# Kernel tuning notes

Hardware: AMD Instinct MI355X
Metric: run time of the kernel (lower is better)

Reference implementation:

```python
import jax, jax.numpy as jnp
import numpy as np

N_NODES = 100000
NODES_PER_GRAPH = 200
N_GRAPHS = N_NODES // NODES_PER_GRAPH  # 500
N_EDGES = 3200000
NUM_FEATURES = 128
HIDDEN = 32
K_POOL = 50
NUM_CLASSES = 10
NUM_ITERATIONS = 3


def setup_inputs() -> dict:
    key = jax.random.key(0)
    ks = jax.random.split(key, 12)
    x = jax.random.normal(ks[0], (N_NODES, NUM_FEATURES), dtype=jnp.float32)
    edge_index = jax.random.randint(ks[1], (2, N_EDGES), 0, N_NODES, dtype=jnp.int64)
    batch = (jnp.arange(N_NODES, dtype=jnp.int64) // NODES_PER_GRAPH)
    # GCN weights (glorot-ish scale) + biases
    W1 = jax.random.normal(ks[2], (NUM_FEATURES, HIDDEN), dtype=jnp.float32) * (1.0 / np.sqrt(NUM_FEATURES))
    b1 = jnp.zeros((HIDDEN,), dtype=jnp.float32)
    W2 = jax.random.normal(ks[3], (HIDDEN, HIDDEN), dtype=jnp.float32) * (1.0 / np.sqrt(HIDDEN))
    b2 = jnp.zeros((HIDDEN,), dtype=jnp.float32)
    W3 = jax.random.normal(ks[4], (HIDDEN, HIDDEN), dtype=jnp.float32) * (1.0 / np.sqrt(HIDDEN))
    b3 = jnp.zeros((HIDDEN,), dtype=jnp.float32)
    # Capsule weights: [out_capsules, in_capsules, out_length, in_length]
    Wc1 = jax.random.normal(ks[5], (16, K_POOL, 32, 3 * HIDDEN), dtype=jnp.float32) * 0.05
    Wc2 = jax.random.normal(ks[6], (NUM_CLASSES, 16, 16, 32), dtype=jnp.float32) * 0.05
    return {"x": x, "edge_index": edge_index, "batch": batch,
            "W1": W1, "b1": b1, "W2": W2, "b2": b2, "W3": W3, "b3": b3,
            "Wc1": Wc1, "Wc2": Wc2}


def _gcn_conv(x, W, b, src, dst, mask):
    # PyG GCNConv: remove self-loops already done (mask), add self-loops, sym-normalize.
    h = x @ W  # [N, H]
    deg = jnp.zeros((x.shape[0],), dtype=h.dtype).at[dst].add(mask) + 1.0  # self-loop adds 1
    dinv = jax.lax.rsqrt(deg)
    norm = dinv[src] * dinv[dst] * mask  # [E]
    agg = jnp.zeros_like(h).at[dst].add(norm[:, None] * h[src])
    agg = agg + h * (dinv * dinv)[:, None]  # self-loop contribution h_i / deg_i
    return agg + b


def _squash(s, axis=-1):
    sq = jnp.sum(s * s, axis=axis, keepdims=True)
    return (sq / (1.0 + sq)) * s * jax.lax.rsqrt(sq + 1e-12)


def _capsule_linear(u, W, num_iterations):
    # u: [B, I, in_len]; W: [O, I, out_len, in_len]
    priors = jnp.einsum('oiLl,bil->boiL', W, u)  # [B, O, I, out_len]
    logits = jnp.zeros(priors.shape[:3] + (1,), dtype=priors.dtype)
    for it in range(num_iterations):
        c = jax.nn.softmax(logits, axis=1)             # over out capsules
        s = jnp.sum(c * priors, axis=2)                # [B, O, out_len]
        v = _squash(s)
        if it < num_iterations - 1:
            logits = logits + jnp.sum(priors * v[:, :, None, :], axis=-1, keepdims=True)
    return v


def _global_sort_pool(x, k):
    # x: [N, C], equal-size graphs -> [B, nper, C]; sort desc by last channel, take top-k
    xg = x.reshape(N_GRAPHS, NODES_PER_GRAPH, x.shape[-1])
    order = jnp.argsort(-xg[:, :, -1], axis=1)[:, :k]  # [B, k]
    return jnp.take_along_axis(xg, order[:, :, None], axis=1)  # [B, k, C]


def reference(x, edge_index, batch, W1, b1, W2, b2, W3, b3, Wc1, Wc2):
    src, dst = edge_index[0], edge_index[1]
    mask = (src != dst).astype(x.dtype)  # remove_self_loops
    x1 = jnp.tanh(_gcn_conv(x, W1, b1, src, dst, mask))
    x2 = jnp.tanh(_gcn_conv(x1, W2, b2, src, dst, mask))
    x3 = jnp.tanh(_gcn_conv(x2, W3, b3, src, dst, mask))
    xc = jnp.concatenate([x1, x2, x3], axis=-1)        # [N, 96]
    pooled = _global_sort_pool(xc, K_POOL)             # [B, 50, 96]
    out = _capsule_linear(pooled, Wc1, NUM_ITERATIONS)  # [B, 16, 32]
    out = _capsule_linear(out, Wc2, NUM_ITERATIONS)     # [B, 10, 16]
    return jnp.linalg.norm(out, axis=-1)                # [B, 10]
```

## Files before the change

kernel.cpp:

```cpp
#include <hip/hip_runtime.h>

#define NNODES 100000
#define NEDGES 3200000
#define NPG 200
#define NGRAPH 500
#define FIN 128
#define HID 32
#define KP 50
#define NCLS 10

#define NB1 196
#define BSH 9
#define CHUNK 8192
#define NBLK1 391
#define CAP 17408

__global__ __launch_bounds__(512) void k_place1(const int* __restrict__ src,
                                                const int* __restrict__ dst,
                                                int* __restrict__ cursor,
                                                unsigned* __restrict__ csorted) {
    __shared__ int hist[NB1];
    __shared__ int lstart[NB1];
    __shared__ int base[NB1];
    __shared__ int cnt2[NB1];
    __shared__ int sarr[256];
    __shared__ unsigned buf[CHUNK];
    __shared__ int dbuf[CHUNK];
    int t = threadIdx.x;
    for (int i = t; i < NB1; i += 512) { hist[i] = 0; cnt2[i] = 0; }
    __syncthreads();
    int eb = blockIdx.x * CHUNK;
    for (int i = 0; i < CHUNK / 512; ++i) {
        int e = eb + t + i * 512;
        if (e < NEDGES) {
            int s = src[e], d = dst[e];
            if (s != d) atomicAdd(&hist[d >> BSH], 1);
        }
    }
    __syncthreads();
    if (t < 256) sarr[t] = (t < NB1) ? hist[t] : 0;
    __syncthreads();
    for (int ofs = 1; ofs < 256; ofs <<= 1) {
        int add = (t < 256 && t >= ofs) ? sarr[t - ofs] : 0;
        __syncthreads();
        if (t < 256) sarr[t] += add;
        __syncthreads();
    }
    if (t < NB1) {
        lstart[t] = (t == 0) ? 0 : sarr[t - 1];
        base[t] = hist[t] ? (t * CAP + atomicAdd(&cursor[t], hist[t])) : 0;
    }
    __syncthreads();
    for (int i = 0; i < CHUNK / 512; ++i) {
        int e = eb + t + i * 512;
        if (e < NEDGES) {
            int s = src[e], d = dst[e];
            if (s != d) {
                int bk = d >> BSH;
                int pos = atomicAdd(&cnt2[bk], 1);
                int slot = lstart[bk] + pos;
                buf[slot] = ((unsigned)s << BSH) | (unsigned)(d & 511);
                dbuf[slot] = base[bk] + pos;
            }
        }
    }
    __syncthreads();
    int nval = sarr[NB1 - 1];
    for (int j = t; j < nval; j += 512) csorted[dbuf[j]] = buf[j];
}

__global__ __launch_bounds__(512) void k_fill2(const int* __restrict__ cursor,
                                               const unsigned* __restrict__ csorted,
                                               int* __restrict__ csrc,
                                               int2* __restrict__ begend,
                                               float* __restrict__ dinv) {
    __shared__ int cnt[512];
    __shared__ int loffs[512];
    __shared__ int cnt2[512];
    __shared__ int sarr[512];
    int b = blockIdx.x, t = threadIdx.x;
    cnt[t] = 0; cnt2[t] = 0;
    __syncthreads();
    int base = b * CAP;
    int m = cursor[b];
    for (int j = t; j < m; j += 512) atomicAdd(&cnt[csorted[base + j] & 511], 1);
    __syncthreads();
    sarr[t] = cnt[t];
    __syncthreads();
    for (int ofs = 1; ofs < 512; ofs <<= 1) {
        int add = (t >= ofs) ? sarr[t - ofs] : 0;
        __syncthreads();
        sarr[t] += add;
        __syncthreads();
    }
    loffs[t] = sarr[t] - cnt[t];
    __syncthreads();
    int n = b * 512 + t;
    if (n < NNODES) {
        int beg = base + loffs[t];
        begend[n] = make_int2(beg, beg + cnt[t]);
        dinv[n] = rsqrtf((float)cnt[t] + 1.0f);
    }
    for (int j = t; j < m; j += 512) {
        unsigned p = csorted[base + j];
        int d = p & 511;
        int pos = atomicAdd(&cnt2[d], 1);
        csrc[base + loffs[d] + pos] = (int)(p >> BSH);
    }
}

__global__ __launch_bounds__(256) void k_matmul(const float* __restrict__ X, int ldx, int K,
                                                const float* __restrict__ W,
                                                const float* __restrict__ dinv,
                                                float* __restrict__ h) {
    __shared__ float Wl[FIN * HID];
    __shared__ float Xl[64 * FIN];
    int t = threadIdx.x;
    for (int idx = t; idx < K * HID; idx += 256) Wl[idx] = W[idx];
    int n0 = blockIdx.x * 64;
    int ng = 64 * K / 4;
    for (int idx = t; idx < ng; idx += 256) {
        int r = (idx * 4) / K, c = (idx * 4) % K;
        float4 v = make_float4(0.f, 0.f, 0.f, 0.f);
        if (n0 + r < NNODES)
            v = *reinterpret_cast<const float4*>(X + (size_t)(n0 + r) * ldx + c);
        *reinterpret_cast<float4*>(&Xl[r * K + c]) = v;
    }
    __syncthreads();
    int j = t & 31, g = t >> 5;
    const float* xr = &Xl[(g * 8) * K];
    float a0 = 0, a1 = 0, a2 = 0, a3 = 0, a4 = 0, a5 = 0, a6 = 0, a7 = 0;
    for (int k = 0; k < K; ++k) {
        float w = Wl[k * HID + j];
        a0 += w * xr[0 * K + k];
        a1 += w * xr[1 * K + k];
        a2 += w * xr[2 * K + k];
        a3 += w * xr[3 * K + k];
        a4 += w * xr[4 * K + k];
        a5 += w * xr[5 * K + k];
        a6 += w * xr[6 * K + k];
        a7 += w * xr[7 * K + k];
    }
    int r0 = n0 + g * 8;
    float av[8] = {a0, a1, a2, a3, a4, a5, a6, a7};
    for (int q = 0; q < 8; ++q)
        if (r0 + q < NNODES) h[(size_t)(r0 + q) * HID + j] = av[q] * dinv[r0 + q];
}

__global__ __launch_bounds__(256) void k_gather(const int2* __restrict__ begend,
                                                const int* __restrict__ csrc,
                                                const float* __restrict__ dinv,
                                                const float* __restrict__ hw,
                                                const float* __restrict__ bias,
                                                float* __restrict__ xc, int coloff) {
    int t = threadIdx.x;
    int wv = t >> 6;
    int lane = t & 63;
    int nh = lane >> 5;
    int sub = lane & 31;
    int g = sub >> 3;
    int q = sub & 7;
    int n = blockIdx.x * 8 + wv * 2 + nh;
    int2 be = begend[n];
    int beg = be.x, end = be.y, last = end - 1;
    float4 acc = make_float4(0.f, 0.f, 0.f, 0.f);
    for (int e0 = beg + g; e0 < end; e0 += 32) {
#pragma unroll
        for (int j = 0; j < 8; ++j) {
            int e = e0 + 4 * j;
            float mk = (e <= last) ? 1.f : 0.f;
            int s = csrc[min(e, last)];
            float4 hv = *reinterpret_cast<const float4*>(hw + (size_t)s * HID + q * 4);
            acc.x += mk * hv.x; acc.y += mk * hv.y; acc.z += mk * hv.z; acc.w += mk * hv.w;
        }
    }
    for (int m = 8; m <= 16; m <<= 1) {
        acc.x += __shfl_xor(acc.x, m, 64);
        acc.y += __shfl_xor(acc.y, m, 64);
        acc.z += __shfl_xor(acc.z, m, 64);
        acc.w += __shfl_xor(acc.w, m, 64);
    }
    if (g == 0) {
        float di = dinv[n];
        float4 hv = *reinterpret_cast<const float4*>(hw + (size_t)n * HID + q * 4);
        float4 bv = *reinterpret_cast<const float4*>(bias + q * 4);
        float4 v;
        v.x = tanhf(di * (acc.x + hv.x) + bv.x);
        v.y = tanhf(di * (acc.y + hv.y) + bv.y);
        v.z = tanhf(di * (acc.z + hv.z) + bv.z);
        v.w = tanhf(di * (acc.w + hv.w) + bv.w);
        *reinterpret_cast<float4*>(xc + (size_t)n * 96 + coloff + q * 4) = v;
    }
}

__global__ __launch_bounds__(256) void k_sortpool(const float* __restrict__ xc,
                                                  float* __restrict__ pooled) {
    int g = blockIdx.x;
    __shared__ float vals[NPG];
    __shared__ int sel[KP];
    int t = threadIdx.x;
    if (t < NPG) vals[t] = xc[((size_t)g * NPG + t) * 96 + 95];
    __syncthreads();
    if (t < NPG) {
        float v = vals[t];
        int r = 0;
        for (int k = 0; k < NPG; ++k) {
            float vk = vals[k];
            r += (vk > v) || (vk == v && k < t);
        }
        if (r < KP) sel[r] = t;
    }
    __syncthreads();
    for (int idx = t; idx < KP * 24; idx += 256) {
        int r = idx / 24, c4 = (idx % 24) * 4;
        *reinterpret_cast<float4*>(pooled + (size_t)g * KP * 96 + r * 96 + c4) =
            *reinterpret_cast<const float4*>(xc + ((size_t)g * NPG + sel[r]) * 96 + c4);
    }
}

__global__ __launch_bounds__(256) void k_priors1(const float* __restrict__ pooled,
                                                 const float* __restrict__ Wc1,
                                                 float* __restrict__ priors) {
    int bid = blockIdx.x;
    int ct = bid & 3;
    int bt = (bid >> 2) & 3;
    int i = bid >> 4;
    __shared__ float As[48 * 128];
    __shared__ float Bs[48 * 128];
    int t = threadIdx.x;
    int tx = t & 15, ty = t >> 4;
    float4 accL[8], accH[8];
#pragma unroll
    for (int r = 0; r < 8; ++r) {
        accL[r] = make_float4(0.f, 0.f, 0.f, 0.f);
        accH[r] = make_float4(0.f, 0.f, 0.f, 0.f);
    }

    for (int kh = 0; kh < 2; ++kh) {
        int kbase = kh * 48;
        __syncthreads();
        for (int idx = t; idx < 128 * 12; idx += 256) {
            int r = idx / 12, c4 = (idx % 12) * 4;
            int b = bt * 128 + r;
            float4 v = make_float4(0.f, 0.f, 0.f, 0.f);
            if (b < NGRAPH)
                v = *reinterpret_cast<const float4*>(pooled + ((size_t)b * KP + i) * 96 + kbase + c4);
            float vv[4] = {v.x, v.y, v.z, v.w};
#pragma unroll
            for (int j = 0; j < 4; ++j) {
                int k = c4 + j;
                int gp = (r >> 2) ^ ((k >> 2) & 31);
                As[k * 128 + gp * 4 + (r & 3)] = vv[j];
            }
        }
        for (int idx = t; idx < 128 * 12; idx += 256) {
            int c = idx / 12, c4 = (idx % 12) * 4;
            int col = ct * 128 + c;
            const float* wr = Wc1 + (((size_t)(col >> 5) * KP + i) * 32 + (col & 31)) * 96;
            float4 v = *reinterpret_cast<const float4*>(wr + kbase + c4);
            float vv[4] = {v.x, v.y, v.z, v.w};
#pragma unroll
            for (int j = 0; j < 4; ++j) {
                int k = c4 + j;
                int gp = (c >> 2) ^ ((k >> 2) & 31);
                Bs[k * 128 + gp * 4 + (c & 3)] = vv[j];
            }
        }
        __syncthreads();
        for (int k = 0; k < 48; ++k) {
            int key = (k >> 2) & 31;
            float4 a0 = *reinterpret_cast<const float4*>(&As[k * 128 + 4 * ((2 * ty) ^ key)]);
            float4 a1 = *reinterpret_cast<const float4*>(&As[k * 128 + 4 * ((2 * ty + 1) ^ key)]);
            float4 b0 = *reinterpret_cast<const float4*>(&Bs[k * 128 + 4 * ((2 * tx) ^ key)]);
            float4 b1 = *reinterpret_cast<const float4*>(&Bs[k * 128 + 4 * ((2 * tx + 1) ^ key)]);
            float a[8] = {a0.x, a0.y, a0.z, a0.w, a1.x, a1.y, a1.z, a1.w};
#pragma unroll
            for (int r = 0; r < 8; ++r) {
                accL[r].x += a[r] * b0.x;
                accL[r].y += a[r] * b0.y;
                accL[r].z += a[r] * b0.z;
                accL[r].w += a[r] * b0.w;
                accH[r].x += a[r] * b1.x;
                accH[r].y += a[r] * b1.y;
                accH[r].z += a[r] * b1.z;
                accH[r].w += a[r] * b1.w;
            }
        }
    }
    int col = ct * 128 + tx * 8;
    int o = col >> 5, L = col & 31;
#pragma unroll
    for (int rr = 0; rr < 8; ++rr) {
        int b = bt * 128 + ty * 8 + rr;
        if (b < NGRAPH) {
            float* dstp = priors + (((size_t)b * 16 + o) * KP + i) * 32 + L;
            *reinterpret_cast<float4*>(dstp) = accL[rr];
            *reinterpret_cast<float4*>(dstp + 4) = accH[rr];
        }
    }
}

__global__ __launch_bounds__(256) void k_routing1(const float* __restrict__ priors_g,
                                                  float* __restrict__ v_out) {
    int b = blockIdx.x;
    __shared__ float P[16 * KP * 33];
    __shared__ float logits[16 * KP];
    __shared__ float c[16 * KP];
    __shared__ float s[16 * 32];
    __shared__ float v[16 * 32];
    __shared__ float scale[16];
    int t = threadIdx.x;
    const float* pg = priors_g + (size_t)b * (16 * KP * 32);
    for (int idx = t; idx < 16 * KP * 32; idx += 256)
        P[(idx >> 5) * 33 + (idx & 31)] = pg[idx];
    for (int idx = t; idx < 16 * KP; idx += 256) logits[idx] = 0.f;
    __syncthreads();
    for (int it = 0; it < 3; ++it) {
        if (t < KP) {
            float m = -1e30f;
            for (int o = 0; o < 16; ++o) m = fmaxf(m, logits[o * KP + t]);
            float sum = 0.f;
            for (int o = 0; o < 16; ++o) {
                float e = expf(logits[o * KP + t] - m);
                c[o * KP + t] = e;
                sum += e;
            }
            for (int o = 0; o < 16; ++o) c[o * KP + t] /= sum;
        }
        __syncthreads();
        for (int idx = t; idx < 16 * 32; idx += 256) {
            int o = idx >> 5, L = idx & 31;
            float acc = 0.f;
            for (int i = 0; i < KP; ++i) acc += c[o * KP + i] * P[(o * KP + i) * 33 + L];
            s[idx] = acc;
        }
        __syncthreads();
        if (t < 16) {
            float sq = 0.f;
            for (int L = 0; L < 32; ++L) sq += s[t * 32 + L] * s[t * 32 + L];
            scale[t] = (sq / (1.f + sq)) * (1.0f / sqrtf(sq + 1e-12f));
        }
        __syncthreads();
        for (int idx = t; idx < 16 * 32; idx += 256) v[idx] = s[idx] * scale[idx >> 5];
        __syncthreads();
        if (it < 2) {
            for (int idx = t; idx < 16 * KP; idx += 256) {
                int o = idx / KP, i = idx % KP;
                float acc = 0.f;
                for (int L = 0; L < 32; ++L) acc += P[(o * KP + i) * 33 + L] * v[o * 32 + L];
                logits[idx] += acc;
            }
            __syncthreads();
        }
    }
    for (int idx = t; idx < 16 * 32; idx += 256) v_out[(size_t)b * 512 + idx] = v[idx];
}

__global__ __launch_bounds__(256) void k_priors2(const float* __restrict__ v1,
                                                 const float* __restrict__ Wc2,
                                                 float* __restrict__ priors2) {
    int b = blockIdx.x;
    __shared__ float ul[16 * 32];
    int t = threadIdx.x;
    for (int idx = t; idx < 512; idx += 256) ul[idx] = v1[(size_t)b * 512 + idx];
    __syncthreads();
    for (int idx = t; idx < NCLS * 16 * 16; idx += 256) {
        int L = idx & 15, i = (idx >> 4) & 15, o = idx >> 8;
        const float* wr = Wc2 + ((size_t)((o * 16 + i) * 16 + L)) * 32;
        const float* ur = &ul[i * 32];
        float acc = 0.f;
        for (int l = 0; l < 32; ++l) acc += wr[l] * ur[l];
        priors2[(size_t)b * (NCLS * 16 * 16) + idx] = acc;
    }
}

__global__ __launch_bounds__(256) void k_routing2(const float* __restrict__ priors_g,
                                                  float* __restrict__ out) {
    int b = blockIdx.x;
    __shared__ float P[NCLS * 16 * 17];
    __shared__ float logits[NCLS * 16];
    __shared__ float c[NCLS * 16];
    __shared__ float s[NCLS * 16];
    __shared__ float v[NCLS * 16];
    __shared__ float scale[NCLS];
    int t = threadIdx.x;
    const float* pg = priors_g + (size_t)b * (NCLS * 16 * 16);
    for (int idx = t; idx < NCLS * 16 * 16; idx += 256)
        P[(idx >> 4) * 17 + (idx & 15)] = pg[idx];
    for (int idx = t; idx < NCLS * 16; idx += 256) logits[idx] = 0.f;
    __syncthreads();
    for (int it = 0; it < 3; ++it) {
        if (t < 16) {
            float m = -1e30f;
            for (int o = 0; o < NCLS; ++o) m = fmaxf(m, logits[o * 16 + t]);
            float sum = 0.f;
            for (int o = 0; o < NCLS; ++o) {
                float e = expf(logits[o * 16 + t] - m);
                c[o * 16 + t] = e;
                sum += e;
            }
            for (int o = 0; o < NCLS; ++o) c[o * 16 + t] /= sum;
        }
        __syncthreads();
        if (t < NCLS * 16) {
            int o = t >> 4, L = t & 15;
            float acc = 0.f;
            for (int i = 0; i < 16; ++i) acc += c[o * 16 + i] * P[(o * 16 + i) * 17 + L];
            s[t] = acc;
        }
        __syncthreads();
        if (t < NCLS) {
            float sq = 0.f;
            for (int L = 0; L < 16; ++L) sq += s[t * 16 + L] * s[t * 16 + L];
            scale[t] = (sq / (1.f + sq)) * (1.0f / sqrtf(sq + 1e-12f));
        }
        __syncthreads();
        if (t < NCLS * 16) v[t] = s[t] * scale[t >> 4];
        __syncthreads();
        if (it < 2) {
            if (t < NCLS * 16) {
                int o = t >> 4, i = t & 15;
                float acc = 0.f;
                for (int L = 0; L < 16; ++L) acc += P[(o * 16 + i) * 17 + L] * v[o * 16 + L];
                logits[t] += acc;
            }
            __syncthreads();
        }
    }
    if (t < NCLS) {
        float sq = 0.f;
        for (int L = 0; L < 16; ++L) sq += v[t * 16 + L] * v[t * 16 + L];
        out[(size_t)b * NCLS + t] = sqrtf(sq);
    }
}

extern "C" void kernel_launch(void* const* d_in, const int* in_sizes, int n_in,
                              void* d_out, int out_size, void* d_ws, size_t ws_size,
                              hipStream_t stream) {
    const float* x   = (const float*)d_in[0];
    const int*   ei  = (const int*)d_in[1];
    const float* W1  = (const float*)d_in[3];
    const float* b1  = (const float*)d_in[4];
    const float* W2  = (const float*)d_in[5];
    const float* b2  = (const float*)d_in[6];
    const float* W3  = (const float*)d_in[7];
    const float* b3  = (const float*)d_in[8];
    const float* Wc1 = (const float*)d_in[9];
    const float* Wc2 = (const float*)d_in[10];
    float* out = (float*)d_out;
    float* wsf = (float*)d_ws;

    const int* src = ei;
    const int* dst = ei + NEDGES;

    float* xc = wsf;
    float* R  = wsf + 9600000;
    int*   cursor  = (int*)R;
    float* dinv    = R + 256;
    int2*  begend  = (int2*)(R + 100256);
    float* A       = R + 300256;
    unsigned* csorted = (unsigned*)A;
    float* h       = A;
    float* pooled  = A;
    int*   csrc    = (int*)(R + 3712224);
    float* pr1     = R + 7124192;
    float* v1      = R + 19924192;
    float* pr2     = R + 20180192;

    hipMemsetAsync(cursor, 0, 256 * sizeof(int), stream);
    k_place1<<<NBLK1, 512, 0, stream>>>(src, dst, cursor, csorted);
    k_fill2<<<NB1, 512, 0, stream>>>(cursor, csorted, csrc, begend, dinv);

    k_matmul<<<(NNODES + 63) / 64, 256, 0, stream>>>(x, FIN, FIN, W1, dinv, h);
    k_gather<<<NNODES / 8, 256, 0, stream>>>(begend, csrc, dinv, h, b1, xc, 0);
    k_matmul<<<(NNODES + 63) / 64, 256, 0, stream>>>(xc, 96, HID, W2, dinv, h);
    k_gather<<<NNODES / 8, 256, 0, stream>>>(begend, csrc, dinv, h, b2, xc, 32);
    k_matmul<<<(NNODES + 63) / 64, 256, 0, stream>>>(xc + 32, 96, HID, W3, dinv, h);
    k_gather<<<NNODES / 8, 256, 0, stream>>>(begend, csrc, dinv, h, b3, xc, 64);

    k_sortpool<<<NGRAPH, 256, 0, stream>>>(xc, pooled);
    k_priors1<<<KP * 16, 256, 0, stream>>>(pooled, Wc1, pr1);
    k_routing1<<<NGRAPH, 256, 0, stream>>>(pr1, v1);
    k_priors2<<<NGRAPH, 256, 0, stream>>>(v1, Wc2, pr2);
    k_routing2<<<NGRAPH, 256, 0, stream>>>(pr2, out);
}
```

Measured before the change: 403.2 us.

## Fuse second capsule priors into routing kernel and remap priors1 thread tiles

Merges the second-layer capsule priors computation into its routing kernel, so priors are built directly in shared memory and the global priors2 buffer plus one launch go away. The inner dot product now uses float4 loads. Separately, the capsule-1 priors GEMM changes its per-thread fragment mapping from adjacent 8-wide groups to two 4-wide groups spaced 64 apart. This is meant to reduce LDS bank conflicts and give more contiguous float4 stores to the priors array. The fused kernel recomputes nothing extra but does more work per block before routing starts.

```diff
diff --git a/kernel.cpp b/kernel.cpp
--- a/kernel.cpp
+++ b/kernel.cpp
@@ -269,10 +269,10 @@
         __syncthreads();
         for (int k = 0; k < 48; ++k) {
             int key = (k >> 2) & 31;
-            float4 a0 = *reinterpret_cast<const float4*>(&As[k * 128 + 4 * ((2 * ty) ^ key)]);
-            float4 a1 = *reinterpret_cast<const float4*>(&As[k * 128 + 4 * ((2 * ty + 1) ^ key)]);
-            float4 b0 = *reinterpret_cast<const float4*>(&Bs[k * 128 + 4 * ((2 * tx) ^ key)]);
-            float4 b1 = *reinterpret_cast<const float4*>(&Bs[k * 128 + 4 * ((2 * tx + 1) ^ key)]);
+            float4 a0 = *reinterpret_cast<const float4*>(&As[k * 128 + 4 * (ty ^ key)]);
+            float4 a1 = *reinterpret_cast<const float4*>(&As[k * 128 + 4 * ((16 + ty) ^ key)]);
+            float4 b0 = *reinterpret_cast<const float4*>(&Bs[k * 128 + 4 * (tx ^ key)]);
+            float4 b1 = *reinterpret_cast<const float4*>(&Bs[k * 128 + 4 * ((16 + tx) ^ key)]);
             float a[8] = {a0.x, a0.y, a0.z, a0.w, a1.x, a1.y, a1.z, a1.w};
 #pragma unroll
             for (int r = 0; r < 8; ++r) {
@@ -287,17 +287,19 @@
             }
         }
     }
-    int col = ct * 128 + tx * 8;
-    int o = col >> 5, L = col & 31;
-#pragma unroll
-    for (int rr = 0; rr < 8; ++rr) {
-        int b = bt * 128 + ty * 8 + rr;
-        if (b < NGRAPH) {
-            float* dstp = priors + (((size_t)b * 16 + o) * KP + i) * 32 + L;
-            *reinterpret_cast<float4*>(dstp) = accL[rr];
-            *reinterpret_cast<float4*>(dstp + 4) = accH[rr];
-        }
-    }
+    int colL = ct * 128 + tx * 4;
+    int colH = colL + 64;
+    int oL = colL >> 5, LL = colL & 31;
+    int oH = colH >> 5, LH = colH & 31;
+#pragma unroll
+    for (int rh = 0; rh < 2; ++rh)
+#pragma unroll
+        for (int j = 0; j < 4; ++j) {
+            int b = bt * 128 + rh * 64 + ty * 4 + j;
+            if (b >= NGRAPH) continue;
+            *reinterpret_cast<float4*>(priors + (((size_t)b * 16 + oL) * KP + i) * 32 + LL) = accL[rh * 4 + j];
+            *reinterpret_cast<float4*>(priors + (((size_t)b * 16 + oH) * KP + i) * 32 + LH) = accH[rh * 4 + j];
+        }
 }
 
 __global__ __launch_bounds__(256) void k_routing1(const float* __restrict__ priors_g,
@@ -356,27 +358,11 @@
     for (int idx = t; idx < 16 * 32; idx += 256) v_out[(size_t)b * 512 + idx] = v[idx];
 }
 
-__global__ __launch_bounds__(256) void k_priors2(const float* __restrict__ v1,
-                                                 const float* __restrict__ Wc2,
-                                                 float* __restrict__ priors2) {
+__global__ __launch_bounds__(256) void k_caps2(const float* __restrict__ v1,
+                                               const float* __restrict__ Wc2,
+                                               float* __restrict__ out) {
     int b = blockIdx.x;
     __shared__ float ul[16 * 32];
-    int t = threadIdx.x;
-    for (int idx = t; idx < 512; idx += 256) ul[idx] = v1[(size_t)b * 512 + idx];
-    __syncthreads();
-    for (int idx = t; idx < NCLS * 16 * 16; idx += 256) {
-        int L = idx & 15, i = (idx >> 4) & 15, o = idx >> 8;
-        const float* wr = Wc2 + ((size_t)((o * 16 + i) * 16 + L)) * 32;
-        const float* ur = &ul[i * 32];
-        float acc = 0.f;
-        for (int l = 0; l < 32; ++l) acc += wr[l] * ur[l];
-        priors2[(size_t)b * (NCLS * 16 * 16) + idx] = acc;
-    }
-}
-
-__global__ __launch_bounds__(256) void k_routing2(const float* __restrict__ priors_g,
-                                                  float* __restrict__ out) {
-    int b = blockIdx.x;
     __shared__ float P[NCLS * 16 * 17];
     __shared__ float logits[NCLS * 16];
     __shared__ float c[NCLS * 16];
@@ -384,10 +370,21 @@
     __shared__ float v[NCLS * 16];
     __shared__ float scale[NCLS];
     int t = threadIdx.x;
-    const float* pg = priors_g + (size_t)b * (NCLS * 16 * 16);
-    for (int idx = t; idx < NCLS * 16 * 16; idx += 256)
-        P[(idx >> 4) * 17 + (idx & 15)] = pg[idx];
+    for (int idx = t; idx < 512; idx += 256) ul[idx] = v1[(size_t)b * 512 + idx];
     for (int idx = t; idx < NCLS * 16; idx += 256) logits[idx] = 0.f;
+    __syncthreads();
+    for (int idx = t; idx < NCLS * 16 * 16; idx += 256) {
+        int L = idx & 15, i = (idx >> 4) & 15, o = idx >> 8;
+        const float4* wr = reinterpret_cast<const float4*>(Wc2 + ((size_t)((o * 16 + i) * 16 + L)) * 32);
+        const float4* ur = reinterpret_cast<const float4*>(&ul[i * 32]);
+        float acc = 0.f;
+#pragma unroll
+        for (int l = 0; l < 8; ++l) {
+            float4 w4 = wr[l], u4 = ur[l];
+            acc += w4.x * u4.x + w4.y * u4.y + w4.z * u4.z + w4.w * u4.w;
+        }
+        P[(idx >> 4) * 17 + L] = acc;
+    }
     __syncthreads();
     for (int it = 0; it < 3; ++it) {
         if (t < 16) {
@@ -465,7 +462,6 @@
     int*   csrc    = (int*)(R + 3712224);
     float* pr1     = R + 7124192;
     float* v1      = R + 19924192;
-    float* pr2     = R + 20180192;
 
     hipMemsetAsync(cursor, 0, 256 * sizeof(int), stream);
     k_place1<<<NBLK1, 512, 0, stream>>>(src, dst, cursor, csorted);
@@ -481,6 +477,5 @@
     k_sortpool<<<NGRAPH, 256, 0, stream>>>(xc, pooled);
     k_priors1<<<KP * 16, 256, 0, stream>>>(pooled, Wc1, pr1);
     k_routing1<<<NGRAPH, 256, 0, stream>>>(pr1, v1);
-    k_priors2<<<NGRAPH, 256, 0, stream>>>(v1, Wc2, pr2);
-    k_routing2<<<NGRAPH, 256, 0, stream>>>(pr2, out);
-}
+    k_caps2<<<NGRAPH, 256, 0, stream>>>(v1, Wc2, out);
+}
```

New measurement: 396.8 us. No clear change (-1.6%).
